# Optimization experiments

Measured on AMD Instinct MI355X. Metric: run time of the kernel, lower is better.

Reference implementation:

```python
import jax, jax.numpy as jnp
import numpy as np

SEQ, FEAT, HID, TGT = 4096, 2048, 2048, 1


def setup_inputs() -> dict:
    key = jax.random.key(0)
    ks = jax.random.split(key, 7)
    s = 1.0 / np.sqrt(HID)  # torch LSTM/Linear default init scale
    return {
        "frame_sequence": jax.random.normal(ks[0], (1, SEQ, FEAT), jnp.float32),
        "W_ih": jax.random.uniform(ks[1], (4 * HID, FEAT), jnp.float32, -s, s),
        "W_hh": jax.random.uniform(ks[2], (4 * HID, HID), jnp.float32, -s, s),
        "b_ih": jax.random.uniform(ks[3], (4 * HID,), jnp.float32, -s, s),
        "b_hh": jax.random.uniform(ks[4], (4 * HID,), jnp.float32, -s, s),
        "W_lin": jax.random.uniform(ks[5], (TGT, HID), jnp.float32, -s, s),
        "b_lin": jax.random.uniform(ks[6], (TGT,), jnp.float32, -s, s),
    }


def reference(frame_sequence, W_ih, W_hh, b_ih, b_hh, W_lin, b_lin):
    H = W_hh.shape[1]
    x = frame_sequence[0]  # [S, F] (module indexes frame_sequence[0])
    # Input-side gate preactivations for ALL timesteps in one GEMM: [S, 4H]
    xg = x @ W_ih.T + (b_ih + b_hh)

    def step(carry, xg_t):
        h, c = carry
        gates = xg_t + h @ W_hh.T  # [4H], torch gate order i,f,g,o
        i, f, g, o = jnp.split(gates, 4)
        i = jax.nn.sigmoid(i)
        f = jax.nn.sigmoid(f)
        g = jnp.tanh(g)
        o = jax.nn.sigmoid(o)
        c = f * c + i * g
        h = o * jnp.tanh(c)
        return (h, c), None

    h0 = jnp.zeros((H,), x.dtype)
    (h_last, _), _ = jax.lax.scan(step, (h0, h0), xg)
    # linear on last hidden state, then sigmoid
    return jax.nn.sigmoid(h_last @ W_lin.T + b_lin)
```

## Files before the change

kernel.cpp:

```cpp
#include <hip/hip_runtime.h>

typedef __attribute__((ext_vector_type(8))) short short8;
typedef __attribute__((ext_vector_type(4))) float f32x4;
typedef __attribute__((ext_vector_type(4))) unsigned uint32x4;

#define SEQ 4096
#define HID 2048
#define G4  8192
#define NBLK 256

static __device__ __forceinline__ ushort f2bf(float f) {
    unsigned u = __float_as_uint(f);
    u = (u + 0x7fffu + ((u >> 16) & 1u)) >> 16;
    return (ushort)u;
}

static __device__ __forceinline__ void atomic_pub_u64(unsigned long long* p,
                                                      unsigned long long v) {
    unsigned long long ap = (unsigned long long)p;
    asm volatile("global_atomic_swap_x2 %0, %1, off" :: "v"(ap), "v"(v) : "memory");
}

static __device__ __forceinline__ void load_slot8(const unsigned long long* p,
                                                  uint32x4& a, uint32x4& b) {
    unsigned long long ap = (unsigned long long)p;
    asm volatile("global_load_dwordx4 %0, %2, off sc0 sc1\n\t"
                 "global_load_dwordx4 %1, %2, off offset:16 sc0 sc1\n\t"
                 "s_waitcnt vmcnt(0)"
                 : "=&v"(a), "=&v"(b) : "v"(ap) : "memory");
}

__global__ void __launch_bounds__(256) k_f32_to_bf16(const float* __restrict__ in,
                                                     ushort* __restrict__ out, int n4) {
    int i = blockIdx.x * blockDim.x + threadIdx.x;
    if (i < n4) {
        float4 v = ((const float4*)in)[i];
        ushort4 o;
        o.x = f2bf(v.x); o.y = f2bf(v.y); o.z = f2bf(v.z); o.w = f2bf(v.w);
        ((ushort4*)out)[i] = o;
    }
}

__global__ void __launch_bounds__(256) k_gemm_xg(
    const ushort* __restrict__ A, const ushort* __restrict__ B,
    const float* __restrict__ bih, const float* __restrict__ bhh,
    float* __restrict__ C)
{
    __shared__ ushort Asm[128 * 40];
    __shared__ ushort Bsm[128 * 40];
    const int tid = threadIdx.x;
    const int brow = blockIdx.y * 128;
    const int bcol = blockIdx.x * 128;
    const int w = tid >> 6, l = tid & 63;
    const int wm = w >> 1, wn = w & 1;

    f32x4 acc[4][4] = {};

    for (int k0 = 0; k0 < 2048; k0 += 32) {
        __syncthreads();
        #pragma unroll
        for (int i = 0; i < 2; ++i) {
            int q = tid + i * 256;
            int r = q >> 2, kc = q & 3;
            *(uint4*)((char*)Asm + r * 80 + kc * 16) =
                *(const uint4*)(A + (size_t)(brow + r) * 2048 + k0 + kc * 8);
            *(uint4*)((char*)Bsm + r * 80 + kc * 16) =
                *(const uint4*)(B + (size_t)(bcol + r) * 2048 + k0 + kc * 8);
        }
        __syncthreads();

        short8 af[4], bf[4];
        #pragma unroll
        for (int m = 0; m < 4; ++m)
            af[m] = *(const short8*)((char*)Asm + (wm * 64 + m * 16 + (l & 15)) * 80 + (l >> 4) * 16);
        #pragma unroll
        for (int n = 0; n < 4; ++n)
            bf[n] = *(const short8*)((char*)Bsm + (wn * 64 + n * 16 + (l & 15)) * 80 + (l >> 4) * 16);

        #pragma unroll
        for (int m = 0; m < 4; ++m)
            #pragma unroll
            for (int n = 0; n < 4; ++n)
                acc[m][n] = __builtin_amdgcn_mfma_f32_16x16x32_bf16(af[m], bf[n], acc[m][n], 0, 0, 0);
    }

    const int lr = (l >> 4) * 4, lc = l & 15;
    #pragma unroll
    for (int m = 0; m < 4; ++m)
        #pragma unroll
        for (int n = 0; n < 4; ++n) {
            int col = bcol + wn * 64 + n * 16 + lc;
            float bsum = bih[col] + bhh[col];
            #pragma unroll
            for (int r = 0; r < 4; ++r) {
                int rowg = brow + wm * 64 + m * 16 + lr + r;
                C[(size_t)rowg * 8192 + col] = acc[m][n][r] + bsum;
            }
        }
}

__global__ void __launch_bounds__(512, 1) k_lstm_rec(
    const ushort* __restrict__ Whh,
    const float* __restrict__ xg,
    unsigned long long* __restrict__ hslot,
    const float* __restrict__ Wlin,
    const float* __restrict__ blin,
    float* __restrict__ out)
{
    extern __shared__ char smem[];
    ushort* w_lds = (ushort*)smem;
    float*  h_lds = (float*)(smem + 131072);
    float*  g_lds = (float*)(smem + 131072 + 8320);

    const int tid = threadIdx.x;
    const int b   = blockIdx.x;
    const int hbase = b * 8;

    for (int rr = 0; rr < 32; rr += 2) {
        int r = rr + (tid >> 8);
        int e = tid & 255;
        int grow = ((r >> 3) << 11) + hbase + (r & 7);
        ((uint4*)(w_lds + r * 2048))[e] = ((const uint4*)(Whh + (size_t)grow * 2048))[e];
    }

    float c_reg = 0.0f;

    if (tid < 8)
        atomic_pub_u64(&hslot[hbase + tid], 0ull);

    const int row = tid >> 4;
    const int cc  = tid & 15;

    for (int t = 0; t < SEQ; ++t) {
        float xgv0 = 0.f, xgv1 = 0.f, xgv2 = 0.f, xgv3 = 0.f;
        if (tid < 8) {
            const float* xr = xg + (size_t)t * G4 + hbase + tid;
            xgv0 = xr[0]; xgv1 = xr[2048]; xgv2 = xr[4096]; xgv3 = xr[6144];
        }

        {
            const unsigned tgt = (unsigned)t;
            uint32x4 a, bq;
            int spin = 0;
            while (true) {
                load_slot8(hslot + tid * 4, a, bq);
                if (a.y == tgt && a.w == tgt && bq.y == tgt && bq.w == tgt) break;
                if ((++spin & 63) == 0) {
                    unsigned d = __hip_atomic_load((const unsigned*)hslot,
                                                   __ATOMIC_ACQUIRE, __HIP_MEMORY_SCOPE_AGENT);
                    asm volatile("" :: "v"(d));
                } else {
                    __builtin_amdgcn_s_sleep(2);
                }
            }
            int col = tid * 4;
            *(f32x4*)(h_lds + col + ((col >> 8) << 2)) =
                (f32x4){__uint_as_float(a.x), __uint_as_float(a.z),
                        __uint_as_float(bq.x), __uint_as_float(bq.z)};
        }
        __syncthreads();

        float s0 = 0.f, s1 = 0.f, s2 = 0.f, s3 = 0.f;
        const ushort* wrow = w_lds + row * 2048;
        #pragma unroll
        for (int k = 0; k < 16; ++k) {
            int col0 = (cc << 3) + (k << 7);
            uint4 wv = *(const uint4*)(wrow + col0);
            const float* hp = h_lds + col0 + ((col0 >> 8) << 2);
            float4 ha = *(const float4*)hp;
            float4 hb = *(const float4*)(hp + 4);
            s0 += __uint_as_float(wv.x << 16)         * ha.x;
            s1 += __uint_as_float(wv.x & 0xffff0000u) * ha.y;
            s2 += __uint_as_float(wv.y << 16)         * ha.z;
            s3 += __uint_as_float(wv.y & 0xffff0000u) * ha.w;
            s0 += __uint_as_float(wv.z << 16)         * hb.x;
            s1 += __uint_as_float(wv.z & 0xffff0000u) * hb.y;
            s2 += __uint_as_float(wv.w << 16)         * hb.z;
            s3 += __uint_as_float(wv.w & 0xffff0000u) * hb.w;
        }
        float sum = (s0 + s1) + (s2 + s3);
        sum += __shfl_xor(sum, 1);
        sum += __shfl_xor(sum, 2);
        sum += __shfl_xor(sum, 4);
        sum += __shfl_xor(sum, 8);
        if (cc == 0) g_lds[row] = sum;
        __syncthreads();

        if (tid < 8) {
            float gi = g_lds[tid]      + xgv0;
            float gf = g_lds[8 + tid]  + xgv1;
            float gg = g_lds[16 + tid] + xgv2;
            float go = g_lds[24 + tid] + xgv3;
            float si = 1.0f / (1.0f + __expf(-gi));
            float sf = 1.0f / (1.0f + __expf(-gf));
            float tg = tanhf(gg);
            float so = 1.0f / (1.0f + __expf(-go));
            c_reg = sf * c_reg + si * tg;
            float hn = so * tanhf(c_reg);
            unsigned long long pv =
                ((unsigned long long)(unsigned)(t + 1) << 32) |
                (unsigned long long)__float_as_uint(hn);
            atomic_pub_u64(&hslot[hbase + tid], pv);
        }
    }

    if (b == 0) {
        const unsigned tgt = (unsigned)SEQ;
        uint32x4 a, bq;
        int spin = 0;
        while (true) {
            load_slot8(hslot + tid * 4, a, bq);
            if (a.y == tgt && a.w == tgt && bq.y == tgt && bq.w == tgt) break;
            if ((++spin & 63) == 0) {
                unsigned d = __hip_atomic_load((const unsigned*)hslot,
                                               __ATOMIC_ACQUIRE, __HIP_MEMORY_SCOPE_AGENT);
                asm volatile("" :: "v"(d));
            } else {
                __builtin_amdgcn_s_sleep(2);
            }
        }
        const float* wl = Wlin + tid * 4;
        float s = __uint_as_float(a.x)  * wl[0] + __uint_as_float(a.z)  * wl[1]
                + __uint_as_float(bq.x) * wl[2] + __uint_as_float(bq.z) * wl[3];
        #pragma unroll
        for (int o = 1; o < 64; o <<= 1) s += __shfl_xor(s, o);
        if ((tid & 63) == 0) g_lds[tid >> 6] = s;
        __syncthreads();
        if (tid == 0) {
            float tot = g_lds[0] + g_lds[1] + g_lds[2] + g_lds[3]
                      + g_lds[4] + g_lds[5] + g_lds[6] + g_lds[7] + blin[0];
            out[0] = 1.0f / (1.0f + __expf(-tot));
        }
    }
}

extern "C" void kernel_launch(void* const* d_in, const int* in_sizes, int n_in,
                              void* d_out, int out_size, void* d_ws, size_t ws_size,
                              hipStream_t stream) {
    const float* x    = (const float*)d_in[0];
    const float* Wih  = (const float*)d_in[1];
    const float* Whh  = (const float*)d_in[2];
    const float* bih  = (const float*)d_in[3];
    const float* bhh  = (const float*)d_in[4];
    const float* Wlin = (const float*)d_in[5];
    const float* blin = (const float*)d_in[6];
    float* out = (float*)d_out;

    char* ws = (char*)d_ws;
    float*              xgbuf = (float*)ws;
    ushort*             xbf   = (ushort*)(ws + 134217728);
    ushort*             wihbf = (ushort*)(ws + 150994944);
    ushort*             whhbf = (ushort*)(ws + 184549376);
    unsigned long long* hslot = (unsigned long long*)(ws + 218103808);

    k_f32_to_bf16<<<8192,  256, 0, stream>>>(x,   xbf,   2097152);
    k_f32_to_bf16<<<16384, 256, 0, stream>>>(Wih, wihbf, 4194304);
    k_f32_to_bf16<<<16384, 256, 0, stream>>>(Whh, whhbf, 4194304);

    k_gemm_xg<<<dim3(64, 32), 256, 0, stream>>>(xbf, wihbf, bih, bhh, xgbuf);

    hipMemsetAsync(hslot, 0xFF, HID * sizeof(unsigned long long), stream);

    hipFuncSetAttribute((const void*)k_lstm_rec,
                        hipFuncAttributeMaxDynamicSharedMemorySize, 163840);
    void* args[] = { (void*)&whhbf, (void*)&xgbuf, (void*)&hslot,
                     (void*)&Wlin, (void*)&blin, (void*)&out };
    hipLaunchCooperativeKernel((const void*)k_lstm_rec, dim3(NBLK), dim3(512),
                               args, 139520, stream);
}
```

Baseline: 14.85 ms.

## Keep W_hh slices in fp32 registers and fuse gate reduction via wave shuffles

The recurrent kernel now converts each block's W_hh rows to fp32 once and keeps them in 128 VGPRs per thread, instead of reading bf16 weights from LDS and unpacking them at every timestep. Each wave now owns one hidden unit with its four gates. The gate sums are combined with shuffles, and every lane computes the cell update, which removes the LDS gate buffer, a barrier, and the serial tid<8 xg loads. The h slots are double-buffered by timestep parity, and the h LDS padding pattern is changed. The cost is very high register pressure and a barrier moved to the end of each step.

```diff
diff --git a/kernel.cpp b/kernel.cpp
--- a/kernel.cpp
+++ b/kernel.cpp
@@ -14,6 +14,8 @@
     u = (u + 0x7fffu + ((u >> 16) & 1u)) >> 16;
     return (ushort)u;
 }
+static __device__ __forceinline__ float bf_lo(unsigned x) { return __uint_as_float(x << 16); }
+static __device__ __forceinline__ float bf_hi(unsigned x) { return __uint_as_float(x & 0xffff0000u); }
 
 static __device__ __forceinline__ void atomic_pub_u64(unsigned long long* p,
                                                       unsigned long long v) {
@@ -29,6 +31,8 @@
                  "s_waitcnt vmcnt(0)"
                  : "=&v"(a), "=&v"(b) : "v"(ap) : "memory");
 }
+
+static __device__ __forceinline__ int hmap(int col) { return col + ((col >> 5) << 2); }
 
 __global__ void __launch_bounds__(256) k_f32_to_bf16(const float* __restrict__ in,
                                                      ushort* __restrict__ out, int n4) {
@@ -108,19 +112,25 @@
     float* __restrict__ out)
 {
     extern __shared__ char smem[];
-    ushort* w_lds = (ushort*)smem;
-    float*  h_lds = (float*)(smem + 131072);
-    float*  g_lds = (float*)(smem + 131072 + 8320);
+    float* h_lds = (float*)smem;
+    float* r_lds = (float*)(smem + 9216);
 
     const int tid = threadIdx.x;
     const int b   = blockIdx.x;
     const int hbase = b * 8;
-
-    for (int rr = 0; rr < 32; rr += 2) {
-        int r = rr + (tid >> 8);
-        int e = tid & 255;
-        int grow = ((r >> 3) << 11) + hbase + (r & 7);
-        ((uint4*)(w_lds + r * 2048))[e] = ((const uint4*)(Whh + (size_t)grow * 2048))[e];
+    const int u  = tid >> 6;
+    const int g  = (tid >> 4) & 3;
+    const int cc = tid & 15;
+
+    f32x4 wf[32];
+    {
+        const ushort* wr = Whh + (size_t)((g << 11) + hbase + u) * 2048 + (cc << 3);
+        #pragma unroll
+        for (int k = 0; k < 16; ++k) {
+            uint4 wv = *(const uint4*)(wr + (k << 7));
+            wf[2 * k]     = (f32x4){bf_lo(wv.x), bf_hi(wv.x), bf_lo(wv.y), bf_hi(wv.y)};
+            wf[2 * k + 1] = (f32x4){bf_lo(wv.z), bf_hi(wv.z), bf_lo(wv.w), bf_hi(wv.w)};
+        }
     }
 
     float c_reg = 0.0f;
@@ -128,80 +138,72 @@
     if (tid < 8)
         atomic_pub_u64(&hslot[hbase + tid], 0ull);
 
-    const int row = tid >> 4;
-    const int cc  = tid & 15;
-
     for (int t = 0; t < SEQ; ++t) {
-        float xgv0 = 0.f, xgv1 = 0.f, xgv2 = 0.f, xgv3 = 0.f;
-        if (tid < 8) {
-            const float* xr = xg + (size_t)t * G4 + hbase + tid;
-            xgv0 = xr[0]; xgv1 = xr[2048]; xgv2 = xr[4096]; xgv3 = xr[6144];
-        }
+        const unsigned long long* src = hslot + (size_t)(t & 1) * HID;
+        unsigned long long*       dst = hslot + (size_t)((t + 1) & 1) * HID;
+
+        float xgv = xg[(size_t)t * G4 + (g << 11) + hbase + u];
 
         {
             const unsigned tgt = (unsigned)t;
             uint32x4 a, bq;
             int spin = 0;
             while (true) {
-                load_slot8(hslot + tid * 4, a, bq);
+                load_slot8(src + tid * 4, a, bq);
                 if (a.y == tgt && a.w == tgt && bq.y == tgt && bq.w == tgt) break;
                 if ((++spin & 63) == 0) {
-                    unsigned d = __hip_atomic_load((const unsigned*)hslot,
+                    unsigned d = __hip_atomic_load((const unsigned*)src,
                                                    __ATOMIC_ACQUIRE, __HIP_MEMORY_SCOPE_AGENT);
                     asm volatile("" :: "v"(d));
                 } else {
                     __builtin_amdgcn_s_sleep(2);
                 }
             }
-            int col = tid * 4;
-            *(f32x4*)(h_lds + col + ((col >> 8) << 2)) =
+            *(f32x4*)(h_lds + hmap(tid * 4)) =
                 (f32x4){__uint_as_float(a.x), __uint_as_float(a.z),
                         __uint_as_float(bq.x), __uint_as_float(bq.z)};
         }
         __syncthreads();
 
         float s0 = 0.f, s1 = 0.f, s2 = 0.f, s3 = 0.f;
-        const ushort* wrow = w_lds + row * 2048;
         #pragma unroll
         for (int k = 0; k < 16; ++k) {
             int col0 = (cc << 3) + (k << 7);
-            uint4 wv = *(const uint4*)(wrow + col0);
-            const float* hp = h_lds + col0 + ((col0 >> 8) << 2);
-            float4 ha = *(const float4*)hp;
-            float4 hb = *(const float4*)(hp + 4);
-            s0 += __uint_as_float(wv.x << 16)         * ha.x;
-            s1 += __uint_as_float(wv.x & 0xffff0000u) * ha.y;
-            s2 += __uint_as_float(wv.y << 16)         * ha.z;
-            s3 += __uint_as_float(wv.y & 0xffff0000u) * ha.w;
-            s0 += __uint_as_float(wv.z << 16)         * hb.x;
-            s1 += __uint_as_float(wv.z & 0xffff0000u) * hb.y;
-            s2 += __uint_as_float(wv.w << 16)         * hb.z;
-            s3 += __uint_as_float(wv.w & 0xffff0000u) * hb.w;
+            const float* hp = h_lds + hmap(col0);
+            f32x4 ha = *(const f32x4*)hp;
+            f32x4 hb = *(const f32x4*)(hp + 4);
+            f32x4 wa = wf[2 * k], wb = wf[2 * k + 1];
+            s0 += wa.x * ha.x;  s1 += wa.y * ha.y;
+            s2 += wa.z * ha.z;  s3 += wa.w * ha.w;
+            s0 += wb.x * hb.x;  s1 += wb.y * hb.y;
+            s2 += wb.z * hb.z;  s3 += wb.w * hb.w;
         }
         float sum = (s0 + s1) + (s2 + s3);
         sum += __shfl_xor(sum, 1);
         sum += __shfl_xor(sum, 2);
         sum += __shfl_xor(sum, 4);
         sum += __shfl_xor(sum, 8);
-        if (cc == 0) g_lds[row] = sum;
-        __syncthreads();
-
-        if (tid < 8) {
-            float gi = g_lds[tid]      + xgv0;
-            float gf = g_lds[8 + tid]  + xgv1;
-            float gg = g_lds[16 + tid] + xgv2;
-            float go = g_lds[24 + tid] + xgv3;
-            float si = 1.0f / (1.0f + __expf(-gi));
-            float sf = 1.0f / (1.0f + __expf(-gf));
-            float tg = tanhf(gg);
-            float so = 1.0f / (1.0f + __expf(-go));
-            c_reg = sf * c_reg + si * tg;
-            float hn = so * tanhf(c_reg);
+        sum += xgv;
+
+        float gi = __shfl(sum, 0);
+        float gf = __shfl(sum, 16);
+        float gg = __shfl(sum, 32);
+        float go = __shfl(sum, 48);
+
+        float si = 1.0f / (1.0f + __expf(-gi));
+        float sf = 1.0f / (1.0f + __expf(-gf));
+        float tg = tanhf(gg);
+        float so = 1.0f / (1.0f + __expf(-go));
+        c_reg = sf * c_reg + si * tg;
+        float hn = so * tanhf(c_reg);
+
+        if ((tid & 63) == 0) {
             unsigned long long pv =
                 ((unsigned long long)(unsigned)(t + 1) << 32) |
                 (unsigned long long)__float_as_uint(hn);
-            atomic_pub_u64(&hslot[hbase + tid], pv);
-        }
+            atomic_pub_u64(&dst[hbase + u], pv);
+        }
+        __syncthreads();
     }
 
     if (b == 0) {
@@ -224,11 +226,11 @@
                 + __uint_as_float(bq.x) * wl[2] + __uint_as_float(bq.z) * wl[3];
         #pragma unroll
         for (int o = 1; o < 64; o <<= 1) s += __shfl_xor(s, o);
-        if ((tid & 63) == 0) g_lds[tid >> 6] = s;
+        if ((tid & 63) == 0) r_lds[u] = s;
         __syncthreads();
         if (tid == 0) {
-            float tot = g_lds[0] + g_lds[1] + g_lds[2] + g_lds[3]
-                      + g_lds[4] + g_lds[5] + g_lds[6] + g_lds[7] + blin[0];
+            float tot = r_lds[0] + r_lds[1] + r_lds[2] + r_lds[3]
+                      + r_lds[4] + r_lds[5] + r_lds[6] + r_lds[7] + blin[0];
             out[0] = 1.0f / (1.0f + __expf(-tot));
         }
     }
@@ -259,7 +261,7 @@
 
     k_gemm_xg<<<dim3(64, 32), 256, 0, stream>>>(xbf, wihbf, bih, bhh, xgbuf);
 
-    hipMemsetAsync(hslot, 0xFF, HID * sizeof(unsigned long long), stream);
+    hipMemsetAsync(hslot, 0xFF, 2 * HID * sizeof(unsigned long long), stream);
 
     hipFuncSetAttribute((const void*)k_lstm_rec,
                         hipFuncAttributeMaxDynamicSharedMemorySize, 163840);
```

Result: slower. 17.96 ms (+20.9%).
